# Kernel tuning notes

Hardware: AMD Instinct MI355X
Metric: run time of the kernel (lower is better)

Reference implementation:

```python
import jax, jax.numpy as jnp
import numpy as np

N_WORDS_BATCH = 16384   # words in the forward batch
EMB_DIM = 128
NUM_ROOTS = 2048
VOCAB = 65536
BOOST = 1.5             # attention_boost_factor
EPS = 1e-8


def setup_inputs() -> dict:
    key = jax.random.key(0)
    k0, k1, k2, k3, k4 = jax.random.split(key, 5)
    word_indices = jax.random.randint(k0, (N_WORDS_BATCH,), 0, VOCAB, dtype=jnp.int32)
    root_map = jax.random.randint(k1, (VOCAB,), 0, NUM_ROOTS, dtype=jnp.int32)
    attention_weights = jax.random.uniform(k2, (N_WORDS_BATCH,), dtype=jnp.float32)
    # kaiming_uniform-like init scale
    root_embeddings = jax.random.normal(k3, (NUM_ROOTS, EMB_DIM), dtype=jnp.float32) / np.sqrt(EMB_DIM).astype(np.float32)
    morpho_transforms = jax.random.normal(k4, (NUM_ROOTS, EMB_DIM, EMB_DIM), dtype=jnp.float32) / np.sqrt(EMB_DIM).astype(np.float32)
    root_bias = jnp.zeros((NUM_ROOTS, EMB_DIM), dtype=jnp.float32)
    return {
        'root_embeddings': root_embeddings,
        'morpho_transforms': morpho_transforms,
        'root_bias': root_bias,
        'attention_weights': attention_weights,
        'word_indices': word_indices,
        'root_map': root_map,
    }


def reference(root_embeddings, morpho_transforms, root_bias, attention_weights, word_indices, root_map):
    num_roots = root_embeddings.shape[0]
    roots = root_map[word_indices]                      # (N,) extract_roots

    # extract_equivariant_features: root-indexed gather + per-root matvec
    embs = root_embeddings[roots]                       # (N, D)
    mats = morpho_transforms[roots]                     # (N, D, D)
    feats = jnp.einsum('nij,nj->ni', mats, embs) + root_bias[roots]

    # compute_root_invariant: segment mean over same-root words, gathered back
    ones = jnp.ones(roots.shape, feats.dtype)
    counts = jax.ops.segment_sum(ones, roots, num_segments=num_roots)      # (R,)
    sums = jax.ops.segment_sum(feats, roots, num_segments=num_roots)       # (R, D)
    inv = (sums / jnp.maximum(counts, 1.0)[:, None])[roots]                # (N, D)

    # boost_attention: weight i is multiplied by BOOST once per other word sharing its root,
    # i.e. w_i * BOOST**(count[root_i] - 1), then softmax(log(w + eps)) over the batch.
    c = counts[roots] - 1.0
    boosted = attention_weights * jnp.power(jnp.float32(BOOST), c)
    boosted = jax.nn.softmax(jnp.log(boosted + EPS))

    return inv * boosted[:, None]
```

## Files before the change

kernel.cpp:

```cpp
#include <hip/hip_runtime.h>

#define N_WORDS 16384
#define EMB 128
#define NROOTS 2048
#define EPS 1e-8f
#define LOG2_BOOST 0.5849625007211562f

#define MV_BLOCKS 32768
#define HIST_BLOCKS 64


__global__ void k_fused(const float* __restrict__ M, const float* __restrict__ e,
                        const float* __restrict__ bias, float* __restrict__ g,
                        const int* __restrict__ wi, const int* __restrict__ rmap,
                        const float* __restrict__ w,
                        int* __restrict__ roots, int* __restrict__ counts,
                        int* __restrict__ done, float* __restrict__ denom) {
    if (blockIdx.x >= MV_BLOCKS) {
        __shared__ int amLast;
        __shared__ float scount[NROOTS];
        __shared__ float sred[4];
        int n = (blockIdx.x - MV_BLOCKS) * 256 + threadIdx.x;
        int r = rmap[wi[n]];
        roots[n] = r;
        atomicAdd(&counts[r], 1);
        __threadfence();
        __syncthreads();
        if (threadIdx.x == 0) amLast = (atomicAdd(done, 1) == HIST_BLOCKS - 1);
        __syncthreads();
        if (!amLast) return;
        __threadfence();
        for (int i = threadIdx.x; i < NROOTS; i += 256)
            scount[i] = (float)(counts[i] - 1);
        __syncthreads();
        float acc = 0.f;
        for (int i = threadIdx.x; i < N_WORDS; i += 256)
            acc += fmaf(w[i], exp2f(scount[roots[i]] * LOG2_BOOST), EPS);
#pragma unroll
        for (int off = 32; off; off >>= 1) acc += __shfl_xor(acc, off, 64);
        int wave = threadIdx.x >> 6, lane = threadIdx.x & 63;
        if (lane == 0) sred[wave] = acc;
        __syncthreads();
        if (threadIdx.x == 0) *denom = sred[0] + sred[1] + sred[2] + sred[3];
        return;
    }
    int b = blockIdx.x;
    int r = b >> 4;
    int wave = threadIdx.x >> 6;
    int lane = threadIdx.x & 63;
    int row = ((b & 15) << 3) + (wave << 1) + (lane >> 5);
    int col = (lane & 31) << 2;
    size_t rbase = (size_t)r << 7;
    const float4 m  = *(const float4*)(M + (rbase + row) * EMB + col);
    const float4 ee = *(const float4*)(e + rbase + col);
    float acc = fmaf(m.x, ee.x, fmaf(m.y, ee.y, fmaf(m.z, ee.z, m.w * ee.w)));
#pragma unroll
    for (int off = 16; off; off >>= 1) acc += __shfl_xor(acc, off, 64);
    if ((lane & 31) == 0) g[rbase + row] = acc + bias[rbase + row];
}

__global__ void k_out(const float* __restrict__ g, const int* __restrict__ roots,
                      const int* __restrict__ counts, const float* __restrict__ w,
                      const float* __restrict__ denom, float4* __restrict__ out) {
    int idx = blockIdx.x * 256 + threadIdx.x;
    int n = idx >> 5;
    int r = roots[n];
    float c = (float)(counts[r] - 1);
    float v = fmaf(w[n], exp2f(c * LOG2_BOOST), EPS);
    float s = v / *denom;
    float4 gv = ((const float4*)(g + ((size_t)r << 7)))[idx & 31];
    gv.x *= s; gv.y *= s; gv.z *= s; gv.w *= s;
    out[idx] = gv;
}

extern "C" void kernel_launch(void* const* d_in, const int* in_sizes, int n_in,
                              void* d_out, int out_size, void* d_ws, size_t ws_size,
                              hipStream_t stream) {
    const float* emb  = (const float*)d_in[0];
    const float* M    = (const float*)d_in[1];
    const float* bias = (const float*)d_in[2];
    const float* attw = (const float*)d_in[3];
    const int*   wi   = (const int*)d_in[4];
    const int*   rmap = (const int*)d_in[5];
    float* out = (float*)d_out;

    char* ws = (char*)d_ws;
    int*   counts = (int*)(ws);
    int*   done   = (int*)(ws + 8192);
    float* denom  = (float*)(ws + 8196);
    int*   roots  = (int*)(ws + 16384);
    float* g      = (float*)(ws + 81920);

    hipMemsetAsync(ws, 0, 8200, stream);
    k_fused<<<MV_BLOCKS + HIST_BLOCKS, 256, 0, stream>>>(M, emb, bias, g, wi, rmap, attw,
                                                         roots, counts, done, denom);
    k_out<<<N_WORDS * (EMB / 4) / 256, 256, 0, stream>>>(g, roots, counts, attw, denom, (float4*)out);
}
```

Before: 237.9 us.

## Assign one block per root for matvec and schedule histogram blocks first

The matvec is restructured from 32768 tiny blocks, each computing 8 rows, to 2048 blocks that each process a whole 128x128 root matrix over 16 iterations, with the embedding vector loaded once per block. The histogram blocks move to the front of the grid so they are dispatched early, and the last histogram block now reads counts directly from global memory instead of staging them in shared memory, with an unrolled loop. This cuts block launch overhead and repeated embedding loads, but gives fewer, longer blocks with less memory-level parallelism per block.

```diff
diff --git a/kernel.cpp b/kernel.cpp
--- a/kernel.cpp
+++ b/kernel.cpp
@@ -5,8 +5,6 @@
 #define NROOTS 2048
 #define EPS 1e-8f
 #define LOG2_BOOST 0.5849625007211562f
-
-#define MV_BLOCKS 32768
 #define HIST_BLOCKS 64
 
 
@@ -16,11 +14,10 @@
                         const float* __restrict__ w,
                         int* __restrict__ roots, int* __restrict__ counts,
                         int* __restrict__ done, float* __restrict__ denom) {
-    if (blockIdx.x >= MV_BLOCKS) {
+    if (blockIdx.x < HIST_BLOCKS) {
         __shared__ int amLast;
-        __shared__ float scount[NROOTS];
         __shared__ float sred[4];
-        int n = (blockIdx.x - MV_BLOCKS) * 256 + threadIdx.x;
+        int n = blockIdx.x * 256 + threadIdx.x;
         int r = rmap[wi[n]];
         roots[n] = r;
         atomicAdd(&counts[r], 1);
@@ -30,12 +27,12 @@
         __syncthreads();
         if (!amLast) return;
         __threadfence();
-        for (int i = threadIdx.x; i < NROOTS; i += 256)
-            scount[i] = (float)(counts[i] - 1);
-        __syncthreads();
         float acc = 0.f;
-        for (int i = threadIdx.x; i < N_WORDS; i += 256)
-            acc += fmaf(w[i], exp2f(scount[roots[i]] * LOG2_BOOST), EPS);
+#pragma unroll 8
+        for (int i = threadIdx.x; i < N_WORDS; i += 256) {
+            float c = (float)(counts[roots[i]] - 1);
+            acc += fmaf(w[i], exp2f(c * LOG2_BOOST), EPS);
+        }
 #pragma unroll
         for (int off = 32; off; off >>= 1) acc += __shfl_xor(acc, off, 64);
         int wave = threadIdx.x >> 6, lane = threadIdx.x & 63;
@@ -44,19 +41,21 @@
         if (threadIdx.x == 0) *denom = sred[0] + sred[1] + sred[2] + sred[3];
         return;
     }
-    int b = blockIdx.x;
-    int r = b >> 4;
-    int wave = threadIdx.x >> 6;
-    int lane = threadIdx.x & 63;
-    int row = ((b & 15) << 3) + (wave << 1) + (lane >> 5);
-    int col = (lane & 31) << 2;
+    int r = blockIdx.x - HIST_BLOCKS;
+    int half = threadIdx.x >> 5;
+    int lane32 = threadIdx.x & 31;
     size_t rbase = (size_t)r << 7;
-    const float4 m  = *(const float4*)(M + (rbase + row) * EMB + col);
-    const float4 ee = *(const float4*)(e + rbase + col);
-    float acc = fmaf(m.x, ee.x, fmaf(m.y, ee.y, fmaf(m.z, ee.z, m.w * ee.w)));
+    const float4* Mr = (const float4*)(M + rbase * EMB);
+    float4 ev = ((const float4*)(e + rbase))[lane32];
 #pragma unroll
-    for (int off = 16; off; off >>= 1) acc += __shfl_xor(acc, off, 64);
-    if ((lane & 31) == 0) g[rbase + row] = acc + bias[rbase + row];
+    for (int it = 0; it < 16; ++it) {
+        int row = (it << 3) + half;
+        float4 m = Mr[(row << 5) + lane32];
+        float d = fmaf(m.x, ev.x, fmaf(m.y, ev.y, fmaf(m.z, ev.z, m.w * ev.w)));
+#pragma unroll
+        for (int off = 16; off; off >>= 1) d += __shfl_xor(d, off, 64);
+        if (lane32 == 0) g[rbase + row] = d + bias[rbase + row];
+    }
 }
 
 __global__ void k_out(const float* __restrict__ g, const int* __restrict__ roots,
@@ -92,7 +91,7 @@
     float* g      = (float*)(ws + 81920);
 
     hipMemsetAsync(ws, 0, 8200, stream);
-    k_fused<<<MV_BLOCKS + HIST_BLOCKS, 256, 0, stream>>>(M, emb, bias, g, wi, rmap, attw,
-                                                         roots, counts, done, denom);
+    k_fused<<<HIST_BLOCKS + NROOTS, 256, 0, stream>>>(M, emb, bias, g, wi, rmap, attw,
+                                                      roots, counts, done, denom);
     k_out<<<N_WORDS * (EMB / 4) / 256, 256, 0, stream>>>(g, roots, counts, attw, denom, (float4*)out);
 }
```

Result: no change. 238.8 us (+0.4%).

## Compute root histogram in a single block with shared-memory atomics, drop memset

Applied to the files above, without the earlier changes.

Replaces the 64 histogram blocks, which used global atomics and a last-block-done counter, with one block that builds the root histogram in shared memory and then computes the softmax denominator. This removes the hipMemsetAsync launch and the global atomic and threadfence traffic. In exchange a single block must process all 16384 words serially, and it is the last block scheduled after 32768 matvec blocks, so it may become a tail on the critical path.

```diff
diff --git a/kernel.cpp b/kernel.cpp
--- a/kernel.cpp
+++ b/kernel.cpp
@@ -7,7 +7,6 @@
 #define LOG2_BOOST 0.5849625007211562f
 
 #define MV_BLOCKS 32768
-#define HIST_BLOCKS 64
 
 
 __global__ void k_fused(const float* __restrict__ M, const float* __restrict__ e,
@@ -15,33 +14,33 @@
                         const int* __restrict__ wi, const int* __restrict__ rmap,
                         const float* __restrict__ w,
                         int* __restrict__ roots, int* __restrict__ counts,
-                        int* __restrict__ done, float* __restrict__ denom) {
-    if (blockIdx.x >= MV_BLOCKS) {
-        __shared__ int amLast;
-        __shared__ float scount[NROOTS];
+                        float* __restrict__ denom) {
+    if (blockIdx.x == MV_BLOCKS) {
+        __shared__ int hcount[NROOTS];
         __shared__ float sred[4];
-        int n = (blockIdx.x - MV_BLOCKS) * 256 + threadIdx.x;
-        int r = rmap[wi[n]];
-        roots[n] = r;
-        atomicAdd(&counts[r], 1);
-        __threadfence();
+        int t = threadIdx.x;
+        for (int i = t; i < NROOTS; i += 256) hcount[i] = 0;
         __syncthreads();
-        if (threadIdx.x == 0) amLast = (atomicAdd(done, 1) == HIST_BLOCKS - 1);
+        for (int i = t; i < N_WORDS; i += 256) {
+            int r = rmap[wi[i]];
+            roots[i] = r;
+            atomicAdd(&hcount[r], 1);
+        }
         __syncthreads();
-        if (!amLast) return;
-        __threadfence();
-        for (int i = threadIdx.x; i < NROOTS; i += 256)
-            scount[i] = (float)(counts[i] - 1);
-        __syncthreads();
+        for (int i = t; i < NROOTS; i += 256) counts[i] = hcount[i];
         float acc = 0.f;
-        for (int i = threadIdx.x; i < N_WORDS; i += 256)
-            acc += fmaf(w[i], exp2f(scount[roots[i]] * LOG2_BOOST), EPS);
+#pragma unroll 8
+        for (int i = t; i < N_WORDS; i += 256) {
+            int r = rmap[wi[i]];
+            float c = (float)(hcount[r] - 1);
+            acc += fmaf(w[i], exp2f(c * LOG2_BOOST), EPS);
+        }
 #pragma unroll
         for (int off = 32; off; off >>= 1) acc += __shfl_xor(acc, off, 64);
-        int wave = threadIdx.x >> 6, lane = threadIdx.x & 63;
+        int wave = t >> 6, lane = t & 63;
         if (lane == 0) sred[wave] = acc;
         __syncthreads();
-        if (threadIdx.x == 0) *denom = sred[0] + sred[1] + sred[2] + sred[3];
+        if (t == 0) *denom = sred[0] + sred[1] + sred[2] + sred[3];
         return;
     }
     int b = blockIdx.x;
@@ -86,13 +85,11 @@
 
     char* ws = (char*)d_ws;
     int*   counts = (int*)(ws);
-    int*   done   = (int*)(ws + 8192);
-    float* denom  = (float*)(ws + 8196);
+    float* denom  = (float*)(ws + 8192);
     int*   roots  = (int*)(ws + 16384);
     float* g      = (float*)(ws + 81920);
 
-    hipMemsetAsync(ws, 0, 8200, stream);
-    k_fused<<<MV_BLOCKS + HIST_BLOCKS, 256, 0, stream>>>(M, emb, bias, g, wi, rmap, attw,
-                                                         roots, counts, done, denom);
+    k_fused<<<MV_BLOCKS + 1, 256, 0, stream>>>(M, emb, bias, g, wi, rmap, attw,
+                                               roots, counts, denom);
     k_out<<<N_WORDS * (EMB / 4) / 256, 256, 0, stream>>>(g, roots, counts, attw, denom, (float4*)out);
 }
```

After: 269.0 us. 1.13x slower.
